# Kernel tuning notes

Measured on AMD Instinct MI355X. Metric: run time of the kernel, lower is better.

Reference implementation:

```python
import jax, jax.numpy as jnp
import numpy as np


def setup_inputs() -> dict:
    key = jax.random.key(0)
    ks = jax.random.split(key, 6)
    B, S, D, G, I, H = 4, 2048, 1024, 256, 1024, 16
    return {
        "inputs_embeds": jax.random.normal(ks[0], (B, S, D), dtype=jnp.float32),
        "structure_features": jax.random.normal(ks[1], (B, G), dtype=jnp.float32),
        "Wq": jax.random.normal(ks[2], (D, I), dtype=jnp.float32) * 0.02,
        "Wk": jax.random.normal(ks[3], (G, I), dtype=jnp.float32) * 0.02,
        "Wv": jax.random.normal(ks[4], (D, I), dtype=jnp.float32) * 0.02,
        "Wo": jax.random.normal(ks[5], (I, D), dtype=jnp.float32) * 0.02,
        "num_heads": 16,
    }


def reference(inputs_embeds, structure_features, Wq, Wk, Wv, Wo, num_heads):
    B, S, D = inputs_embeds.shape
    I = Wq.shape[1]
    H = num_heads
    hd = I // H
    scale = 1.0 / (hd ** 0.5)

    # queries/values from token embeddings: [B, S, I] -> [B, H, S, hd]
    q = (inputs_embeds @ Wq).reshape(B, S, H, hd).transpose(0, 2, 1, 3)
    v = (inputs_embeds @ Wv).reshape(B, S, H, hd).transpose(0, 2, 1, 3)

    # structure_features is repeat-expanded to seq_len in the original; the
    # projection of identical rows is identical, so project once and broadcast.
    k1 = (structure_features @ Wk).reshape(B, 1, H, hd).transpose(0, 2, 1, 3)  # [B, H, 1, hd]
    k = jnp.broadcast_to(k1, (B, H, S, hd))  # same values as key_proj(repeated sf)

    # [B, H, S, S] score matrix (columns identical by construction, as in the
    # original module) -> softmax -> weighted sum of values.
    scores = jnp.einsum("bhqd,bhkd->bhqk", q, k) * scale
    probs = jax.nn.softmax(scores, axis=-1)
    attended = jnp.einsum("bhqk,bhkd->bhqd", probs, v)  # [B, H, S, hd]

    attended = attended.transpose(0, 2, 1, 3).reshape(B, S, I)
    return attended @ Wo
```

## Files before the change

kernel.cpp:

```cpp
#include <hip/hip_runtime.h>

#define BB 4
#define SS 2048
#define DD 1024
#define II 1024


constexpr int JP = 128;
constexpr int ROWS1 = SS / JP;

__global__ __launch_bounds__(256)
void k1_partial(const float4* __restrict__ x, float4* __restrict__ pbuf) {
    const int g = blockIdx.x;
    const float4* xr = x + (size_t)g * ROWS1 * (DD / 4) + threadIdx.x;
    float4 a = make_float4(0.f, 0.f, 0.f, 0.f);
    #pragma unroll
    for (int r = 0; r < ROWS1; ++r) {
        float4 v = xr[(size_t)r * (DD / 4)];
        a.x += v.x; a.y += v.y; a.z += v.z; a.w += v.w;
    }
    pbuf[(size_t)g * (DD / 4) + threadIdx.x] = a;
}

__global__ __launch_bounds__(256)
void kred(const float4* __restrict__ pbuf, float4* __restrict__ xbar) {
    const int b = blockIdx.x >> 4, dg = blockIdx.x & 15;
    const int c4 = threadIdx.x & 15;
    const int jg = threadIdx.x >> 4;
    const float4* p = pbuf + ((size_t)b * JP + jg * 8) * (DD / 4) + dg * 16 + c4;
    float4 a = make_float4(0.f, 0.f, 0.f, 0.f);
    #pragma unroll
    for (int j = 0; j < 8; ++j) {
        float4 v = p[(size_t)j * (DD / 4)];
        a.x += v.x; a.y += v.y; a.z += v.z; a.w += v.w;
    }
    __shared__ float4 red[16][16];
    red[jg][c4] = a;
    __syncthreads();
    if (threadIdx.x < 16) {
        float4 s = make_float4(0.f, 0.f, 0.f, 0.f);
        #pragma unroll
        for (int q = 0; q < 16; ++q) {
            float4 v = red[q][threadIdx.x];
            s.x += v.x; s.y += v.y; s.z += v.z; s.w += v.w;
        }
        const float sc = 1.0f / (float)SS;
        xbar[b * (DD / 4) + dg * 16 + threadIdx.x] =
            make_float4(s.x * sc, s.y * sc, s.z * sc, s.w * sc);
    }
}

__global__ __launch_bounds__(1024)
void kg_gemv(const float4* __restrict__ vec, const float* __restrict__ W,
             float* __restrict__ out) {
    __shared__ float xs[BB * DD];
    const int tid = threadIdx.x;
    ((float4*)xs)[tid] = vec[tid];
    __syncthreads();

    const int i0 = blockIdx.x * 16;
    const int il = tid & 15, ks = tid >> 4;
    float a0 = 0.f, a1 = 0.f, a2 = 0.f, a3 = 0.f;
    #pragma unroll
    for (int kk = 0; kk < 16; ++kk) {
        const int k = ks * 16 + kk;
        const float w = W[(size_t)k * DD + i0 + il];
        a0 += xs[0 * DD + k] * w;
        a1 += xs[1 * DD + k] * w;
        a2 += xs[2 * DD + k] * w;
        a3 += xs[3 * DD + k] * w;
    }

    __shared__ float red[64 * 64];
    red[ks * 64 +  0 + il] = a0;
    red[ks * 64 + 16 + il] = a1;
    red[ks * 64 + 32 + il] = a2;
    red[ks * 64 + 48 + il] = a3;
    __syncthreads();
    if (tid < 64) {
        float s = 0.f;
        #pragma unroll
        for (int q = 0; q < 64; ++q) s += red[q * 64 + tid];
        const int b = tid >> 4, i = tid & 15;
        out[b * DD + i0 + i] = s;
    }
}

__global__ __launch_bounds__(256)
void k4_bcast(const float4* __restrict__ orow, float4* __restrict__ out) {
    const int g = blockIdx.x;
    const int b = g >> 9;
    const int s0 = (g & 511) * 4;
    const float4 c = orow[b * (DD / 4) + threadIdx.x];
    float4* o = out + (size_t)(b * SS + s0) * (DD / 4) + threadIdx.x;
    #pragma unroll
    for (int r = 0; r < 4; ++r) o[(size_t)r * (DD / 4)] = c;
}

extern "C" void kernel_launch(void* const* d_in, const int* in_sizes, int n_in,
                              void* d_out, int out_size, void* d_ws, size_t ws_size,
                              hipStream_t stream) {
    const float* x  = (const float*)d_in[0];
    const float* Wv = (const float*)d_in[4];
    const float* Wo = (const float*)d_in[5];
    float* out = (float*)d_out;

    float* pbuf = (float*)d_ws;
    float* xbar = pbuf + (size_t)BB * JP * DD;
    float* tvec = xbar + (size_t)BB * DD;
    float* orow = tvec + (size_t)BB * II;

    k1_partial<<<BB * JP, 256, 0, stream>>>((const float4*)x, (float4*)pbuf);
    kred<<<64, 256, 0, stream>>>((const float4*)pbuf, (float4*)xbar);
    kg_gemv<<<II / 16, 1024, 0, stream>>>((const float4*)xbar, Wv, tvec);
    kg_gemv<<<DD / 16, 1024, 0, stream>>>((const float4*)tvec, Wo, orow);
    k4_bcast<<<(BB * SS) / 4, 256, 0, stream>>>((const float4*)orow, (float4*)out);
}
```

Baseline: 111.0 us.

## Fuse all five stages into one cooperative persistent kernel with grid syncs

Replaces the five separate launches (partial row sums, reduction, two GEMVs, broadcast) with a single cooperative kernel of 512 blocks that uses grid.sync between stages, to remove launch gaps and per-kernel ramp-up. It also switches the input reads and output writes to nontemporal loads and stores, and gives each output-writing block 16 rows instead of 4. The GEMV stages run on only 64 blocks while the rest wait at the barriers. If the cooperative launch fails, the code falls back to the old multi-kernel path.

```diff
diff --git a/kernel.cpp b/kernel.cpp
--- a/kernel.cpp
+++ b/kernel.cpp
@@ -1,4 +1,7 @@
 #include <hip/hip_runtime.h>
+#include <hip/hip_cooperative_groups.h>
+
+namespace cg = cooperative_groups;
 
 #define BB 4
 #define SS 2048
@@ -6,8 +9,117 @@
 #define II 1024
 
 
-constexpr int JP = 128;
+constexpr int NBLK  = 512;
+constexpr int JP    = 128;
 constexpr int ROWS1 = SS / JP;
+constexpr int REDLD = 65;
+
+typedef float f4 __attribute__((ext_vector_type(4)));
+
+__device__ __forceinline__
+void gemv16(const float* __restrict__ vec, const float* __restrict__ W,
+            float* __restrict__ outv, int g, int tid,
+            float* __restrict__ xs, float* __restrict__ red)
+{
+    #pragma unroll
+    for (int r = 0; r < 4; ++r)
+        ((f4*)xs)[tid + 256 * r] = ((const f4*)vec)[tid + 256 * r];
+    __syncthreads();
+
+    const int i0 = g * 16;
+    const int il = tid & 15, ks = tid >> 4;
+    const float* wp = W + (size_t)(ks * 64) * DD + i0 + il;
+    float a0 = 0.f, a1 = 0.f, a2 = 0.f, a3 = 0.f;
+    #pragma unroll 16
+    for (int kk = 0; kk < 64; ++kk) {
+        const float w = wp[(size_t)kk * DD];
+        const int k = ks * 64 + kk;
+        a0 += xs[0 * DD + k] * w;
+        a1 += xs[1 * DD + k] * w;
+        a2 += xs[2 * DD + k] * w;
+        a3 += xs[3 * DD + k] * w;
+    }
+    red[ks * REDLD +  0 + il] = a0;
+    red[ks * REDLD + 16 + il] = a1;
+    red[ks * REDLD + 32 + il] = a2;
+    red[ks * REDLD + 48 + il] = a3;
+    __syncthreads();
+    if (tid < 64) {
+        float s = 0.f;
+        #pragma unroll
+        for (int q = 0; q < 16; ++q) s += red[q * REDLD + tid];
+        const int b = tid >> 4, i = tid & 15;
+        outv[b * DD + i0 + i] = s;
+    }
+    __syncthreads();
+}
+
+__global__ __launch_bounds__(256, 2)
+void fused_all(const float* __restrict__ x,
+               const float* __restrict__ Wv,
+               const float* __restrict__ Wo,
+               float* __restrict__ pbuf,
+               float* __restrict__ xbar,
+               float* __restrict__ tvec,
+               float* __restrict__ orow,
+               float* __restrict__ out)
+{
+    __shared__ float xs[BB * DD];
+    __shared__ float red[16 * REDLD];
+
+    cg::grid_group grid = cg::this_grid();
+    const int g   = blockIdx.x;
+    const int tid = threadIdx.x;
+
+    {
+        const f4* xr = (const f4*)x + (size_t)g * ROWS1 * (DD / 4) + tid;
+        f4 a = (f4)(0.f);
+        #pragma unroll
+        for (int r = 0; r < ROWS1; ++r)
+            a += __builtin_nontemporal_load(xr + (size_t)r * (DD / 4));
+        ((f4*)pbuf)[(size_t)g * (DD / 4) + tid] = a;
+    }
+    grid.sync();
+
+    if (g < 64) {
+        const int b = g >> 4, dg = g & 15;
+        const int c4 = tid & 15;
+        const int jg = tid >> 4;
+        const f4* p = (const f4*)pbuf + ((size_t)b * JP + jg * 8) * (DD / 4)
+                      + dg * 16 + c4;
+        f4 a = (f4)(0.f);
+        #pragma unroll
+        for (int j = 0; j < 8; ++j)
+            a += p[(size_t)j * (DD / 4)];
+        f4* redb = (f4*)xs;
+        redb[jg * 16 + c4] = a;
+        __syncthreads();
+        if (tid < 16) {
+            f4 s = (f4)(0.f);
+            #pragma unroll
+            for (int q = 0; q < 16; ++q) s += redb[q * 16 + tid];
+            ((f4*)xbar)[b * (DD / 4) + dg * 16 + tid] = s * (1.0f / (float)SS);
+        }
+    }
+    grid.sync();
+
+    if (g < 64) gemv16(xbar, Wv, tvec, g, tid, xs, red);
+    grid.sync();
+
+    if (g < 64) gemv16(tvec, Wo, orow, g, tid, xs, red);
+    grid.sync();
+
+    {
+        const int b  = g >> 7;
+        const int s0 = (g & 127) * 16;
+        const f4 c = ((const f4*)orow)[b * (DD / 4) + tid];
+        f4* o = (f4*)out + (size_t)(b * SS + s0) * (DD / 4) + tid;
+        #pragma unroll
+        for (int r = 0; r < 16; ++r)
+            __builtin_nontemporal_store(c, o + (size_t)r * (DD / 4));
+    }
+}
+
 
 __global__ __launch_bounds__(256)
 void k1_partial(const float4* __restrict__ x, float4* __restrict__ pbuf) {
@@ -34,14 +146,14 @@
         float4 v = p[(size_t)j * (DD / 4)];
         a.x += v.x; a.y += v.y; a.z += v.z; a.w += v.w;
     }
-    __shared__ float4 red[16][16];
-    red[jg][c4] = a;
+    __shared__ float4 red2[16][16];
+    red2[jg][c4] = a;
     __syncthreads();
     if (threadIdx.x < 16) {
         float4 s = make_float4(0.f, 0.f, 0.f, 0.f);
         #pragma unroll
         for (int q = 0; q < 16; ++q) {
-            float4 v = red[q][threadIdx.x];
+            float4 v = red2[q][threadIdx.x];
             s.x += v.x; s.y += v.y; s.z += v.z; s.w += v.w;
         }
         const float sc = 1.0f / (float)SS;
@@ -71,16 +183,16 @@
         a3 += xs[3 * DD + k] * w;
     }
 
-    __shared__ float red[64 * 64];
-    red[ks * 64 +  0 + il] = a0;
-    red[ks * 64 + 16 + il] = a1;
-    red[ks * 64 + 32 + il] = a2;
-    red[ks * 64 + 48 + il] = a3;
+    __shared__ float red3[64 * 64];
+    red3[ks * 64 +  0 + il] = a0;
+    red3[ks * 64 + 16 + il] = a1;
+    red3[ks * 64 + 32 + il] = a2;
+    red3[ks * 64 + 48 + il] = a3;
     __syncthreads();
     if (tid < 64) {
         float s = 0.f;
         #pragma unroll
-        for (int q = 0; q < 64; ++q) s += red[q * 64 + tid];
+        for (int q = 0; q < 64; ++q) s += red3[q * 64 + tid];
         const int b = tid >> 4, i = tid & 15;
         out[b * DD + i0 + i] = s;
     }
@@ -106,13 +218,22 @@
     float* out = (float*)d_out;
 
     float* pbuf = (float*)d_ws;
-    float* xbar = pbuf + (size_t)BB * JP * DD;
+    float* xbar = pbuf + (size_t)NBLK * DD;
     float* tvec = xbar + (size_t)BB * DD;
     float* orow = tvec + (size_t)BB * II;
 
-    k1_partial<<<BB * JP, 256, 0, stream>>>((const float4*)x, (float4*)pbuf);
-    kred<<<64, 256, 0, stream>>>((const float4*)pbuf, (float4*)xbar);
-    kg_gemv<<<II / 16, 1024, 0, stream>>>((const float4*)xbar, Wv, tvec);
-    kg_gemv<<<DD / 16, 1024, 0, stream>>>((const float4*)tvec, Wo, orow);
-    k4_bcast<<<(BB * SS) / 4, 256, 0, stream>>>((const float4*)orow, (float4*)out);
-}
+    void* args[] = { (void*)&x, (void*)&Wv, (void*)&Wo,
+                     (void*)&pbuf, (void*)&xbar, (void*)&tvec, (void*)&orow,
+                     (void*)&out };
+    hipError_t err = hipLaunchCooperativeKernel(
+        reinterpret_cast<void*>(fused_all), dim3(NBLK), dim3(256),
+        args, 0, stream);
+
+    if (err != hipSuccess) {
+        k1_partial<<<BB * JP, 256, 0, stream>>>((const float4*)x, (float4*)pbuf);
+        kred<<<64, 256, 0, stream>>>((const float4*)pbuf, (float4*)xbar);
+        kg_gemv<<<II / 16, 1024, 0, stream>>>((const float4*)xbar, Wv, tvec);
+        kg_gemv<<<DD / 16, 1024, 0, stream>>>((const float4*)tvec, Wo, orow);
+        k4_bcast<<<(BB * SS) / 4, 256, 0, stream>>>((const float4*)orow, (float4*)out);
+    }
+}
```

Result: slower. 337.3 us (+203.8%).
